# Kernel optimization log

Measured on AMD Instinct MI355X. Metric: run time of the kernel, lower is better.

Reference implementation:

```python
import jax, jax.numpy as jnp
import numpy as np

N = 50000      # nodes
E = 600000     # edges
D_IN = 128
D_H = 128
D_OUT = 64


def setup_inputs() -> dict:
    key = jax.random.key(0)
    ks = jax.random.split(key, 10)
    x = jax.random.normal(ks[0], (N, D_IN), dtype=jnp.float32)
    edge_index = jax.random.randint(ks[1], (2, E), 0, N, dtype=jnp.int32)
    def lin(k, fan_out, fan_in):
        s = 1.0 / np.sqrt(fan_in)
        return jax.random.uniform(k, (fan_out, fan_in), jnp.float32, -s, s)
    W0 = lin(ks[2], D_H, D_IN);   b0 = jnp.zeros((D_H,), jnp.float32)
    W1 = lin(ks[3], D_H, D_H);    b1 = jnp.zeros((D_H,), jnp.float32)
    W2 = lin(ks[4], D_H, D_H);    b2 = jnp.zeros((D_H,), jnp.float32)
    W3 = lin(ks[5], D_OUT, D_H);  b3 = jnp.zeros((D_OUT,), jnp.float32)
    return {"x": x, "edge_index": edge_index,
            "W0": W0, "b0": b0, "W1": W1, "b1": b1,
            "W2": W2, "b2": b2, "W3": W3, "b3": b3}


def reference(x, edge_index, W0, b0, W1, b1, W2, b2, W3, b3):
    n = x.shape[0]
    loops = jnp.arange(n, dtype=edge_index.dtype)
    row = jnp.concatenate([edge_index[0], loops])  # sources (with self-loops)
    col = jnp.concatenate([edge_index[1], loops])  # targets
    # symmetric normalization D^-1/2 (A+I) D^-1/2 (PyG GCNConv default)
    deg = jax.ops.segment_sum(jnp.ones(row.shape, x.dtype), col, num_segments=n)
    dinv = jnp.where(deg > 0, jax.lax.rsqrt(deg), 0.0)
    norm = dinv[row] * dinv[col]  # [E+N]

    def gcn_conv(h, W, b):
        h = h @ W.T                              # [n, out]
        msg = h[row] * norm[:, None]             # gather + scale
        out = jax.ops.segment_sum(msg, col, num_segments=n)  # scatter-add
        return out + b

    h = jax.nn.relu(gcn_conv(x, W0, b0))   # Dropout is identity in eval mode
    h = jax.nn.relu(gcn_conv(h, W1, b1))
    h = jax.nn.relu(gcn_conv(h, W2, b2))
    return gcn_conv(h, W3, b3)
```

## Files before the change

kernel.cpp:

```cpp
#include <hip/hip_runtime.h>

#define D_INF 128
#define SLOTCAP 64

typedef __attribute__((ext_vector_type(8))) short bf16x8;
typedef __attribute__((ext_vector_type(4))) float f32x4;
typedef unsigned short u16;
typedef unsigned int   u32;

__device__ inline u16 f2bf(float f) {
    u32 u = __float_as_uint(f);
    u32 r = (u + 0x7fffu + ((u >> 16) & 1u)) >> 16;
    return (u16)r;
}
__device__ inline float bf2f(u16 h) { return __uint_as_float(((u32)h) << 16); }

__global__ void k_fill(const int* __restrict__ rowv, const int* __restrict__ colv,
                       int* __restrict__ fill, int* __restrict__ slots, int E) {
    int e = blockIdx.x * blockDim.x + threadIdx.x;
    if (e >= E) return;
    int c = colv[e];
    int pos = atomicAdd(&fill[c], 1);
    if (pos < SLOTCAP) slots[c * SLOTCAP + pos] = rowv[e];
}

__global__ void k_wfill(const int* __restrict__ fill, const int* __restrict__ slots,
                        const float* __restrict__ dinv, float* __restrict__ wbuf, int N) {
    int i = blockIdx.x * 256 + threadIdx.x;
    if (i >= N * SLOTCAP) return;
    const int node = i >> 6, sl = i & 63;
    const int deg = min(fill[node], SLOTCAP);
    wbuf[i] = (sl < deg) ? dinv[slots[i]] : 0.0f;
}

__global__ void k_split_x(const float* __restrict__ x, u16* __restrict__ Xcat,
                          const int* __restrict__ fill, float* __restrict__ dinv,
                          int Nreal, int Mpad) {
    int idx = blockIdx.x * 256 + threadIdx.x;
    int total = Mpad * 32;
    if (idx >= total) return;
    const int row = idx >> 5, c4 = (idx & 31) * 4;
    if (c4 == 0 && row < Nreal)
        dinv[row] = (float)(1.0 / sqrt((double)(fill[row] + 1)));
    float4 v = make_float4(0.f, 0.f, 0.f, 0.f);
    if (row < Nreal) v = *(const float4*)(x + (size_t)row * 128 + c4);
    u16 h0 = f2bf(v.x), h1 = f2bf(v.y), h2 = f2bf(v.z), h3 = f2bf(v.w);
    u16 l0 = f2bf(v.x - bf2f(h0)), l1 = f2bf(v.y - bf2f(h1));
    u16 l2 = f2bf(v.z - bf2f(h2)), l3 = f2bf(v.w - bf2f(h3));
    u16* dst = Xcat + (size_t)row * 256 + c4;
    *(u32*)(dst)       = (u32)h0 | ((u32)h1 << 16);
    *(u32*)(dst + 2)   = (u32)h2 | ((u32)h3 << 16);
    *(u32*)(dst + 128) = (u32)l0 | ((u32)l1 << 16);
    *(u32*)(dst + 130) = (u32)l2 | ((u32)l3 << 16);
}

__global__ void k_split_w(const float* __restrict__ W0, const float* __restrict__ W1,
                          const float* __restrict__ W2, const float* __restrict__ W3,
                          u16* __restrict__ Wcat) {
    const int l = blockIdx.y;
    const float* W = (l == 0) ? W0 : (l == 1) ? W1 : (l == 2) ? W2 : W3;
    const int rows = (l == 3) ? 64 : 128;
    int idx = blockIdx.x * 256 + threadIdx.x;
    if (idx >= rows * 128) return;
    const int r = idx >> 7, c = idx & 127;
    float v = W[idx];
    u16 h = f2bf(v);
    u16 lo = f2bf(v - bf2f(h));
    u16* dst = Wcat + (size_t)l * 128 * 256 + (size_t)r * 256 + c;
    dst[0]   = h;
    dst[128] = lo;
}

template <int FM>
__global__ __launch_bounds__(256)
void k_gemm_mfma(const u16* __restrict__ Xcat, const u16* __restrict__ Wcat,
                 float* __restrict__ H) {
    constexpr int Dout = (FM == 4) ? 128 : 64;
    const int tid = threadIdx.x;
    const int wave = tid >> 6, lane = tid & 63;
    const int wm = (FM == 4) ? (wave >> 1) : wave;
    const int wn = (FM == 4) ? (wave & 1) : 0;
    const int row_base = blockIdx.x * 128 + wm * (FM * 16);
    const int col_base = wn * 64;
    const int lr = lane & 15;
    const int kg = lane >> 4;

    f32x4 acc[FM][4] = {};

    #pragma unroll 2
    for (int ks = 0; ks < 8; ++ks) {
        const int k0 = ks * 32 + kg * 8;
        bf16x8 a[FM], b[4];
        #pragma unroll
        for (int i = 0; i < FM; ++i)
            a[i] = *(const bf16x8*)(Xcat + (size_t)(row_base + i * 16 + lr) * 256 + k0);
        #pragma unroll
        for (int j = 0; j < 4; ++j)
            b[j] = *(const bf16x8*)(Wcat + (size_t)(col_base + j * 16 + lr) * 256 + k0);
        #pragma unroll
        for (int i = 0; i < FM; ++i)
            #pragma unroll
            for (int j = 0; j < 4; ++j)
                acc[i][j] = __builtin_amdgcn_mfma_f32_16x16x32_bf16(a[i], b[j], acc[i][j], 0, 0, 0);
    }

    #pragma unroll
    for (int i = 0; i < FM; ++i) {
        const int r0 = row_base + i * 16 + kg * 4;
        #pragma unroll
        for (int j = 0; j < 4; ++j) {
            const int c = col_base + j * 16 + lr;
            #pragma unroll
            for (int q = 0; q < 4; ++q)
                H[(size_t)(r0 + q) * Dout + c] = acc[i][j][q];
        }
    }
}

template <int D, int OUT_MODE>
__global__ void k_agg_gather(const float* __restrict__ H, const float* __restrict__ dinv,
                             const int* __restrict__ fill, const int* __restrict__ slots,
                             const float* __restrict__ wbuf, const float* __restrict__ b,
                             void* __restrict__ out, int N) {
    const int node = blockIdx.x * 4 + (threadIdx.x >> 6);
    const int lane = threadIdx.x & 63;
    if (node >= N) return;
    const int deg = min(fill[node], SLOTCAP);
    const float dc = dinv[node];

    int s_l = 0; float w_l = 0.f;
    if (lane < deg) {
        s_l = slots[node * SLOTCAP + lane];
        w_l = wbuf[node * SLOTCAP + lane];
    }
    const int m8 = (deg + 7) & ~7;

    if (D == 128) {
        const int d0 = lane * 2;
        float a0[8] = {}, a1[8] = {};
        {
            const float2 hs = *(const float2*)(H + (size_t)node * D + d0);
            a0[0] = dc * hs.x; a1[0] = dc * hs.y;
        }
        for (int j = 0; j < m8; j += 8) {
            int s[8]; float w[8];
            #pragma unroll
            for (int q = 0; q < 8; ++q) {
                s[q] = __shfl(s_l, j + q);
                w[q] = __shfl(w_l, j + q);
            }
            float2 h[8];
            #pragma unroll
            for (int q = 0; q < 8; ++q)
                h[q] = *(const float2*)(H + (size_t)s[q] * D + d0);
            #pragma unroll
            for (int q = 0; q < 8; ++q) {
                a0[q] = fmaf(w[q], h[q].x, a0[q]);
                a1[q] = fmaf(w[q], h[q].y, a1[q]);
            }
        }
        float A0 = ((a0[0] + a0[1]) + (a0[2] + a0[3])) + ((a0[4] + a0[5]) + (a0[6] + a0[7]));
        float A1 = ((a1[0] + a1[1]) + (a1[2] + a1[3])) + ((a1[4] + a1[5]) + (a1[6] + a1[7]));
        float v0 = fmaf(dc, A0, b[d0]);
        float v1 = fmaf(dc, A1, b[d0 + 1]);
        if (OUT_MODE == 1) {
            v0 = fmaxf(v0, 0.0f); v1 = fmaxf(v1, 0.0f);
            const u16 h0 = f2bf(v0), h1 = f2bf(v1);
            const u16 l0 = f2bf(v0 - bf2f(h0)), l1 = f2bf(v1 - bf2f(h1));
            u16* xc = (u16*)out + (size_t)node * 256 + d0;
            *(u32*)(xc)       = (u32)h0 | ((u32)h1 << 16);
            *(u32*)(xc + 128) = (u32)l0 | ((u32)l1 << 16);
        } else {
            *(float2*)((float*)out + (size_t)node * D + d0) = make_float2(v0, v1);
        }
    } else {
        const int half = lane >> 5;
        const int l32 = lane & 31;
        const int d0 = l32 * 2;
        float a0[4] = {}, a1[4] = {};
        if (half == 0) {
            const float2 hs = *(const float2*)(H + (size_t)node * D + d0);
            a0[0] = dc * hs.x; a1[0] = dc * hs.y;
        }
        for (int j = 0; j < m8; j += 8) {
            int s[4]; float w[4];
            #pragma unroll
            for (int q = 0; q < 4; ++q) {
                const int e = j + 2 * q + half;
                s[q] = __shfl(s_l, e);
                w[q] = __shfl(w_l, e);
            }
            float2 h[4];
            #pragma unroll
            for (int q = 0; q < 4; ++q)
                h[q] = *(const float2*)(H + (size_t)s[q] * D + d0);
            #pragma unroll
            for (int q = 0; q < 4; ++q) {
                a0[q] = fmaf(w[q], h[q].x, a0[q]);
                a1[q] = fmaf(w[q], h[q].y, a1[q]);
            }
        }
        float A0 = (a0[0] + a0[1]) + (a0[2] + a0[3]);
        float A1 = (a1[0] + a1[1]) + (a1[2] + a1[3]);
        A0 += __shfl_xor(A0, 32);
        A1 += __shfl_xor(A1, 32);
        if (half == 0) {
            float v0 = fmaf(dc, A0, b[d0]);
            float v1 = fmaf(dc, A1, b[d0 + 1]);
            *(float2*)((float*)out + (size_t)node * D + d0) = make_float2(v0, v1);
        }
    }
}

extern "C" void kernel_launch(void* const* d_in, const int* in_sizes, int n_in,
                              void* d_out, int out_size, void* d_ws, size_t ws_size,
                              hipStream_t stream) {
    const float* x  = (const float*)d_in[0];
    const int*   ei = (const int*)d_in[1];
    const float* W[4] = {(const float*)d_in[2], (const float*)d_in[4],
                         (const float*)d_in[6], (const float*)d_in[8]};
    const float* B[4] = {(const float*)d_in[3], (const float*)d_in[5],
                         (const float*)d_in[7], (const float*)d_in[9]};
    const int N = in_sizes[0] / D_INF;
    const int E = in_sizes[1] / 2;
    const int Mpad = (N + 127) & ~127;
    const int* rowv = ei;
    const int* colv = ei + E;

    size_t nPad = ((size_t)N + 255) & ~(size_t)255;
    int*   fill  = (int*)d_ws;
    float* dinv  = (float*)(fill + nPad);
    int*   slots = (int*)(dinv + nPad);
    float* wbuf  = (float*)(slots + (size_t)N * SLOTCAP);
    float* Hbuf  = wbuf + (size_t)N * SLOTCAP;
    u16*   Xcat  = (u16*)(Hbuf + (size_t)Mpad * 128);
    u16*   Wcat  = Xcat + (size_t)Mpad * 256;

    const int TB = 256;
    int nbE = (E + TB - 1) / TB;

    hipMemsetAsync(fill, 0, (size_t)N * sizeof(int), stream);
    k_fill<<<nbE, TB, 0, stream>>>(rowv, colv, fill, slots, E);
    k_split_x<<<(Mpad * 32 + TB - 1) / TB, TB, 0, stream>>>(x, Xcat, fill, dinv, N, Mpad);
    k_wfill<<<(N * SLOTCAP + TB - 1) / TB, TB, 0, stream>>>(fill, slots, dinv, wbuf, N);
    {
        dim3 g(64, 4);
        k_split_w<<<g, TB, 0, stream>>>(W[0], W[1], W[2], W[3], Wcat);
    }

    const int aggGrid = (N + 3) / 4;
    const int gemmGrid = Mpad / 128;

    for (int l = 0; l < 3; ++l) {
        k_gemm_mfma<4><<<gemmGrid, 256, 0, stream>>>(Xcat, Wcat + (size_t)l * 128 * 256, Hbuf);
        k_agg_gather<128, 1><<<aggGrid, TB, 0, stream>>>(Hbuf, dinv, fill, slots, wbuf,
                                                         B[l], (void*)Xcat, N);
    }
    k_gemm_mfma<2><<<gemmGrid, 256, 0, stream>>>(Xcat, Wcat + (size_t)3 * 128 * 256, Hbuf);
    k_agg_gather<64, 0><<<aggGrid, TB, 0, stream>>>(Hbuf, dinv, fill, slots, wbuf,
                                                    B[3], d_out, N);
}
```

Before: 299.2 us.

## Fuse aggregation and GEMM per layer using aggregate-then-transform order

Each GCN layer becomes one kernel. It first gathers and normalizes neighbor features into a swizzled shared-memory tile, then multiplies that tile by the weight matrix with bf16 MFMA, adding bias, ReLU and the hi/lo split in the epilogue. This removes the fp32 H intermediate round-trip and half of the kernel launches, and the activations are kept in an interleaved packed hi/lo u32 layout. The cost is that the gather moves 128-wide packed inputs even for the last 64-wide layer. The large shared tile and 512-thread blocks may also reduce occupancy, and the weights are read per block from global memory.

```diff
diff --git a/kernel.cpp b/kernel.cpp
--- a/kernel.cpp
+++ b/kernel.cpp
@@ -1,6 +1,5 @@
 #include <hip/hip_runtime.h>
 
-#define D_INF 128
 #define SLOTCAP 64
 
 typedef __attribute__((ext_vector_type(8))) short bf16x8;
@@ -14,6 +13,14 @@
     return (u16)r;
 }
 __device__ inline float bf2f(u16 h) { return __uint_as_float(((u32)h) << 16); }
+__device__ inline u32 packhl(float f) {
+    u16 h = f2bf(f);
+    u16 l = f2bf(f - bf2f(h));
+    return (u32)h | ((u32)l << 16);
+}
+__device__ inline float unpackhl(u32 u) {
+    return bf2f((u16)u) + bf2f((u16)(u >> 16));
+}
 
 __global__ void k_fill(const int* __restrict__ rowv, const int* __restrict__ colv,
                        int* __restrict__ fill, int* __restrict__ slots, int E) {
@@ -33,7 +40,7 @@
     wbuf[i] = (sl < deg) ? dinv[slots[i]] : 0.0f;
 }
 
-__global__ void k_split_x(const float* __restrict__ x, u16* __restrict__ Xcat,
+__global__ void k_split_x(const float* __restrict__ x, u32* __restrict__ X,
                           const int* __restrict__ fill, float* __restrict__ dinv,
                           int Nreal, int Mpad) {
     int idx = blockIdx.x * 256 + threadIdx.x;
@@ -44,14 +51,9 @@
         dinv[row] = (float)(1.0 / sqrt((double)(fill[row] + 1)));
     float4 v = make_float4(0.f, 0.f, 0.f, 0.f);
     if (row < Nreal) v = *(const float4*)(x + (size_t)row * 128 + c4);
-    u16 h0 = f2bf(v.x), h1 = f2bf(v.y), h2 = f2bf(v.z), h3 = f2bf(v.w);
-    u16 l0 = f2bf(v.x - bf2f(h0)), l1 = f2bf(v.y - bf2f(h1));
-    u16 l2 = f2bf(v.z - bf2f(h2)), l3 = f2bf(v.w - bf2f(h3));
-    u16* dst = Xcat + (size_t)row * 256 + c4;
-    *(u32*)(dst)       = (u32)h0 | ((u32)h1 << 16);
-    *(u32*)(dst + 2)   = (u32)h2 | ((u32)h3 << 16);
-    *(u32*)(dst + 128) = (u32)l0 | ((u32)l1 << 16);
-    *(u32*)(dst + 130) = (u32)l2 | ((u32)l3 << 16);
+    uint4 o;
+    o.x = packhl(v.x); o.y = packhl(v.y); o.z = packhl(v.z); o.w = packhl(v.w);
+    *(uint4*)(X + (size_t)row * 128 + c4) = o;
 }
 
 __global__ void k_split_w(const float* __restrict__ W0, const float* __restrict__ W1,
@@ -71,143 +73,113 @@
     dst[128] = lo;
 }
 
-template <int FM>
-__global__ __launch_bounds__(256)
-void k_gemm_mfma(const u16* __restrict__ Xcat, const u16* __restrict__ Wcat,
-                 float* __restrict__ H) {
-    constexpr int Dout = (FM == 4) ? 128 : 64;
+template <int Dout, int OUT_MODE>
+__global__ __launch_bounds__(512)
+void k_layer(const u32* __restrict__ Xin, const u16* __restrict__ Wc,
+             const float* __restrict__ b, const float* __restrict__ dinv,
+             const int* __restrict__ fill, const int* __restrict__ slots,
+             const float* __restrict__ wbuf, void* __restrict__ out, int N) {
+    __shared__ u16 Asub[64 * 256];
     const int tid = threadIdx.x;
     const int wave = tid >> 6, lane = tid & 63;
-    const int wm = (FM == 4) ? (wave >> 1) : wave;
-    const int wn = (FM == 4) ? (wave & 1) : 0;
-    const int row_base = blockIdx.x * 128 + wm * (FM * 16);
-    const int col_base = wn * 64;
-    const int lr = lane & 15;
-    const int kg = lane >> 4;
-
-    f32x4 acc[FM][4] = {};
-
-    #pragma unroll 2
+    const int node_base = blockIdx.x * 64;
+
+    for (int t = 0; t < 8; ++t) {
+        const int lrow = wave * 8 + t;
+        const int node = node_base + lrow;
+        float Ax = 0.f, Ay = 0.f;
+        const int d0 = lane * 2;
+        if (node < N) {
+            const int deg = min(fill[node], SLOTCAP);
+            const float dc = dinv[node];
+            int s_l = 0; float w_l = 0.f;
+            if (lane < deg) {
+                s_l = slots[node * SLOTCAP + lane];
+                w_l = wbuf[node * SLOTCAP + lane];
+            }
+            float a0[8] = {}, a1[8] = {};
+            {
+                const uint2 sv = *(const uint2*)(Xin + (size_t)node * 128 + d0);
+                a0[0] = dc * unpackhl(sv.x);
+                a1[0] = dc * unpackhl(sv.y);
+            }
+            const int m8 = (deg + 7) & ~7;
+            for (int j = 0; j < m8; j += 8) {
+                int s[8]; float w[8];
+                #pragma unroll
+                for (int q = 0; q < 8; ++q) {
+                    s[q] = __shfl(s_l, j + q);
+                    w[q] = __shfl(w_l, j + q);
+                }
+                uint2 h[8];
+                #pragma unroll
+                for (int q = 0; q < 8; ++q)
+                    h[q] = *(const uint2*)(Xin + (size_t)s[q] * 128 + d0);
+                #pragma unroll
+                for (int q = 0; q < 8; ++q) {
+                    a0[q] = fmaf(w[q], unpackhl(h[q].x), a0[q]);
+                    a1[q] = fmaf(w[q], unpackhl(h[q].y), a1[q]);
+                }
+            }
+            float A0 = ((a0[0] + a0[1]) + (a0[2] + a0[3])) + ((a0[4] + a0[5]) + (a0[6] + a0[7]));
+            float A1 = ((a1[0] + a1[1]) + (a1[2] + a1[3])) + ((a1[4] + a1[5]) + (a1[6] + a1[7]));
+            Ax = dc * A0; Ay = dc * A1;
+        }
+        const u16 h0 = f2bf(Ax), h1 = f2bf(Ay);
+        const u16 l0 = f2bf(Ax - bf2f(h0)), l1 = f2bf(Ay - bf2f(h1));
+        const u32 C = (u32)((lrow & 7) << 4);
+        char* base = (char*)Asub + lrow * 512;
+        *(u32*)(base + ((4 * lane) ^ C))       = (u32)h0 | ((u32)h1 << 16);
+        *(u32*)(base + ((256 + 4 * lane) ^ C)) = (u32)l0 | ((u32)l1 << 16);
+    }
+    __syncthreads();
+
+    constexpr int FM = (Dout == 128) ? 2 : 1;
+    constexpr int FN = 2;
+    const int wm = (Dout == 128) ? (wave >> 2) : (wave >> 1);
+    const int wn = (Dout == 128) ? (wave & 3) : (wave & 1);
+    const int rbase = wm * (FM * 16);
+    const int cbase = wn * (FN * 16);
+    const int lr = lane & 15, kg = lane >> 4;
+
+    f32x4 acc[FM][FN] = {};
+    #pragma unroll
     for (int ks = 0; ks < 8; ++ks) {
-        const int k0 = ks * 32 + kg * 8;
-        bf16x8 a[FM], b[4];
-        #pragma unroll
-        for (int i = 0; i < FM; ++i)
-            a[i] = *(const bf16x8*)(Xcat + (size_t)(row_base + i * 16 + lr) * 256 + k0);
-        #pragma unroll
-        for (int j = 0; j < 4; ++j)
-            b[j] = *(const bf16x8*)(Wcat + (size_t)(col_base + j * 16 + lr) * 256 + k0);
+        bf16x8 a[FM], bw[FN];
+        #pragma unroll
+        for (int i = 0; i < FM; ++i) {
+            const int row = rbase + i * 16 + lr;
+            const int byte = row * 512 + ((ks * 64 + kg * 16) ^ ((row & 7) << 4));
+            a[i] = *(const bf16x8*)((const char*)Asub + byte);
+        }
+        #pragma unroll
+        for (int j = 0; j < FN; ++j)
+            bw[j] = *(const bf16x8*)(Wc + (size_t)(cbase + j * 16 + lr) * 256 + ks * 32 + kg * 8);
         #pragma unroll
         for (int i = 0; i < FM; ++i)
             #pragma unroll
-            for (int j = 0; j < 4; ++j)
-                acc[i][j] = __builtin_amdgcn_mfma_f32_16x16x32_bf16(a[i], b[j], acc[i][j], 0, 0, 0);
+            for (int j = 0; j < FN; ++j)
+                acc[i][j] = __builtin_amdgcn_mfma_f32_16x16x32_bf16(a[i], bw[j], acc[i][j], 0, 0, 0);
     }
 
     #pragma unroll
     for (int i = 0; i < FM; ++i) {
-        const int r0 = row_base + i * 16 + kg * 4;
-        #pragma unroll
-        for (int j = 0; j < 4; ++j) {
-            const int c = col_base + j * 16 + lr;
-            #pragma unroll
-            for (int q = 0; q < 4; ++q)
-                H[(size_t)(r0 + q) * Dout + c] = acc[i][j][q];
-        }
-    }
-}
-
-template <int D, int OUT_MODE>
-__global__ void k_agg_gather(const float* __restrict__ H, const float* __restrict__ dinv,
-                             const int* __restrict__ fill, const int* __restrict__ slots,
-                             const float* __restrict__ wbuf, const float* __restrict__ b,
-                             void* __restrict__ out, int N) {
-    const int node = blockIdx.x * 4 + (threadIdx.x >> 6);
-    const int lane = threadIdx.x & 63;
-    if (node >= N) return;
-    const int deg = min(fill[node], SLOTCAP);
-    const float dc = dinv[node];
-
-    int s_l = 0; float w_l = 0.f;
-    if (lane < deg) {
-        s_l = slots[node * SLOTCAP + lane];
-        w_l = wbuf[node * SLOTCAP + lane];
-    }
-    const int m8 = (deg + 7) & ~7;
-
-    if (D == 128) {
-        const int d0 = lane * 2;
-        float a0[8] = {}, a1[8] = {};
-        {
-            const float2 hs = *(const float2*)(H + (size_t)node * D + d0);
-            a0[0] = dc * hs.x; a1[0] = dc * hs.y;
-        }
-        for (int j = 0; j < m8; j += 8) {
-            int s[8]; float w[8];
-            #pragma unroll
-            for (int q = 0; q < 8; ++q) {
-                s[q] = __shfl(s_l, j + q);
-                w[q] = __shfl(w_l, j + q);
-            }
-            float2 h[8];
-            #pragma unroll
-            for (int q = 0; q < 8; ++q)
-                h[q] = *(const float2*)(H + (size_t)s[q] * D + d0);
-            #pragma unroll
-            for (int q = 0; q < 8; ++q) {
-                a0[q] = fmaf(w[q], h[q].x, a0[q]);
-                a1[q] = fmaf(w[q], h[q].y, a1[q]);
-            }
-        }
-        float A0 = ((a0[0] + a0[1]) + (a0[2] + a0[3])) + ((a0[4] + a0[5]) + (a0[6] + a0[7]));
-        float A1 = ((a1[0] + a1[1]) + (a1[2] + a1[3])) + ((a1[4] + a1[5]) + (a1[6] + a1[7]));
-        float v0 = fmaf(dc, A0, b[d0]);
-        float v1 = fmaf(dc, A1, b[d0 + 1]);
-        if (OUT_MODE == 1) {
-            v0 = fmaxf(v0, 0.0f); v1 = fmaxf(v1, 0.0f);
-            const u16 h0 = f2bf(v0), h1 = f2bf(v1);
-            const u16 l0 = f2bf(v0 - bf2f(h0)), l1 = f2bf(v1 - bf2f(h1));
-            u16* xc = (u16*)out + (size_t)node * 256 + d0;
-            *(u32*)(xc)       = (u32)h0 | ((u32)h1 << 16);
-            *(u32*)(xc + 128) = (u32)l0 | ((u32)l1 << 16);
-        } else {
-            *(float2*)((float*)out + (size_t)node * D + d0) = make_float2(v0, v1);
-        }
-    } else {
-        const int half = lane >> 5;
-        const int l32 = lane & 31;
-        const int d0 = l32 * 2;
-        float a0[4] = {}, a1[4] = {};
-        if (half == 0) {
-            const float2 hs = *(const float2*)(H + (size_t)node * D + d0);
-            a0[0] = dc * hs.x; a1[0] = dc * hs.y;
-        }
-        for (int j = 0; j < m8; j += 8) {
-            int s[4]; float w[4];
+        #pragma unroll
+        for (int j = 0; j < FN; ++j) {
             #pragma unroll
             for (int q = 0; q < 4; ++q) {
-                const int e = j + 2 * q + half;
-                s[q] = __shfl(s_l, e);
-                w[q] = __shfl(w_l, e);
-            }
-            float2 h[4];
-            #pragma unroll
-            for (int q = 0; q < 4; ++q)
-                h[q] = *(const float2*)(H + (size_t)s[q] * D + d0);
-            #pragma unroll
-            for (int q = 0; q < 4; ++q) {
-                a0[q] = fmaf(w[q], h[q].x, a0[q]);
-                a1[q] = fmaf(w[q], h[q].y, a1[q]);
-            }
-        }
-        float A0 = (a0[0] + a0[1]) + (a0[2] + a0[3]);
-        float A1 = (a1[0] + a1[1]) + (a1[2] + a1[3]);
-        A0 += __shfl_xor(A0, 32);
-        A1 += __shfl_xor(A1, 32);
-        if (half == 0) {
-            float v0 = fmaf(dc, A0, b[d0]);
-            float v1 = fmaf(dc, A1, b[d0 + 1]);
-            *(float2*)((float*)out + (size_t)node * D + d0) = make_float2(v0, v1);
+                const int lrow = rbase + i * 16 + kg * 4 + q;
+                const int node = node_base + lrow;
+                if (node >= N) continue;
+                const int col = cbase + j * 16 + lr;
+                float v = acc[i][j][q] + b[col];
+                if (OUT_MODE == 1) {
+                    v = fmaxf(v, 0.0f);
+                    ((u32*)out)[(size_t)node * 128 + col] = packhl(v);
+                } else {
+                    ((float*)out)[(size_t)node * Dout + col] = v;
+                }
+            }
         }
     }
 }
@@ -221,7 +193,7 @@
                          (const float*)d_in[6], (const float*)d_in[8]};
     const float* B[4] = {(const float*)d_in[3], (const float*)d_in[5],
                          (const float*)d_in[7], (const float*)d_in[9]};
-    const int N = in_sizes[0] / D_INF;
+    const int N = in_sizes[0] / 128;
     const int E = in_sizes[1] / 2;
     const int Mpad = (N + 127) & ~127;
     const int* rowv = ei;
@@ -232,31 +204,31 @@
     float* dinv  = (float*)(fill + nPad);
     int*   slots = (int*)(dinv + nPad);
     float* wbuf  = (float*)(slots + (size_t)N * SLOTCAP);
-    float* Hbuf  = wbuf + (size_t)N * SLOTCAP;
-    u16*   Xcat  = (u16*)(Hbuf + (size_t)Mpad * 128);
-    u16*   Wcat  = Xcat + (size_t)Mpad * 256;
+    u32*   XA    = (u32*)(wbuf + (size_t)N * SLOTCAP);
+    u32*   XB    = XA + (size_t)Mpad * 128;
+    u16*   Wcat  = (u16*)(XB + (size_t)Mpad * 128);
 
     const int TB = 256;
     int nbE = (E + TB - 1) / TB;
 
     hipMemsetAsync(fill, 0, (size_t)N * sizeof(int), stream);
     k_fill<<<nbE, TB, 0, stream>>>(rowv, colv, fill, slots, E);
-    k_split_x<<<(Mpad * 32 + TB - 1) / TB, TB, 0, stream>>>(x, Xcat, fill, dinv, N, Mpad);
+    k_split_x<<<(Mpad * 32 + TB - 1) / TB, TB, 0, stream>>>(x, XA, fill, dinv, N, Mpad);
     k_wfill<<<(N * SLOTCAP + TB - 1) / TB, TB, 0, stream>>>(fill, slots, dinv, wbuf, N);
     {
         dim3 g(64, 4);
         k_split_w<<<g, TB, 0, stream>>>(W[0], W[1], W[2], W[3], Wcat);
     }
 
-    const int aggGrid = (N + 3) / 4;
-    const int gemmGrid = Mpad / 128;
-
-    for (int l = 0; l < 3; ++l) {
-        k_gemm_mfma<4><<<gemmGrid, 256, 0, stream>>>(Xcat, Wcat + (size_t)l * 128 * 256, Hbuf);
-        k_agg_gather<128, 1><<<aggGrid, TB, 0, stream>>>(Hbuf, dinv, fill, slots, wbuf,
-                                                         B[l], (void*)Xcat, N);
-    }
-    k_gemm_mfma<2><<<gemmGrid, 256, 0, stream>>>(Xcat, Wcat + (size_t)3 * 128 * 256, Hbuf);
-    k_agg_gather<64, 0><<<aggGrid, TB, 0, stream>>>(Hbuf, dinv, fill, slots, wbuf,
-                                                    B[3], d_out, N);
-}
+    const int lgrid = (N + 63) / 64;
+    const size_t wsl = (size_t)128 * 256;
+
+    k_layer<128, 1><<<lgrid, 512, 0, stream>>>(XA, Wcat + 0 * wsl, B[0], dinv, fill,
+                                               slots, wbuf, (void*)XB, N);
+    k_layer<128, 1><<<lgrid, 512, 0, stream>>>(XB, Wcat + 1 * wsl, B[1], dinv, fill,
+                                               slots, wbuf, (void*)XA, N);
+    k_layer<128, 1><<<lgrid, 512, 0, stream>>>(XA, Wcat + 2 * wsl, B[2], dinv, fill,
+                                               slots, wbuf, (void*)XB, N);
+    k_layer<64, 0><<<lgrid, 512, 0, stream>>>(XB, Wcat + 3 * wsl, B[3], dinv, fill,
+                                              slots, wbuf, d_out, N);
+}
```

Result: slower. 370.9 us (+24.0%).
